# Kernel tuning notes

Measured on AMD Instinct MI355X. Metric: run time of the kernel, lower is better.

Reference implementation:

```python
import jax, jax.numpy as jnp
import numpy as np

N_STATE = 1024
N_HEADS = 16
D_HEAD = N_STATE // N_HEADS
N_CTX = 4080
T_PAD = 128 * 32  # ctx_blks * block_size = 4096
N_RESBLOCKS = 24
LN_EPS = 1e-5


def setup_inputs() -> dict:
    key = jax.random.key(0)
    ks = jax.random.split(key, 12)
    std_qkv = 1.0 / np.sqrt(N_STATE)
    std_c = 1.0 / np.sqrt(N_STATE * N_RESBLOCKS ** 2)
    return {
        "m": jax.random.normal(ks[0], (1, N_CTX, N_STATE), jnp.float32),
        "bias": jax.random.normal(ks[1], (T_PAD, T_PAD), jnp.float32) * 0.1,
        "gamma": jnp.ones((N_STATE,), jnp.float32),
        "beta": jnp.zeros((N_STATE,), jnp.float32),
        "Wq": jax.random.normal(ks[2], (N_STATE, N_STATE), jnp.float32) * std_qkv,
        "bq": jnp.zeros((N_STATE,), jnp.float32),
        "Wk": jax.random.normal(ks[3], (N_STATE, N_STATE), jnp.float32) * std_qkv,
        "Wv": jax.random.normal(ks[4], (N_STATE, N_STATE), jnp.float32) * std_qkv,
        "bv": jnp.zeros((N_STATE,), jnp.float32),
        "Wc": jax.random.normal(ks[5], (N_STATE, N_STATE), jnp.float32) * std_c,
        "bc": jnp.zeros((N_STATE,), jnp.float32),
    }


def reference(m, bias, gamma, beta, Wq, bq, Wk, Wv, bv, Wc, bc):
    B, n_ctx, n_state = m.shape
    n_pad = T_PAD - n_ctx  # same pad for queries and keys here

    # LayerNorm
    mu = jnp.mean(m, axis=-1, keepdims=True)
    var = jnp.mean(jnp.square(m - mu), axis=-1, keepdims=True)
    r = (m - mu) * jax.lax.rsqrt(var + LN_EPS) * gamma + beta

    q = r @ Wq + bq
    k = r @ Wk          # f_k has use_bias=False
    v = r @ Wv + bv

    pad = ((0, 0), (0, n_pad), (0, 0))
    q = jnp.pad(q, pad)
    k = jnp.pad(k, pad)
    v = jnp.pad(v, pad)

    # [B, T_PAD, H, D] -> attention per head
    q = q.reshape(B, T_PAD, N_HEADS, D_HEAD)
    k = k.reshape(B, T_PAD, N_HEADS, D_HEAD)
    v = v.reshape(B, T_PAD, N_HEADS, D_HEAD)

    scale = 1.0 / np.sqrt(D_HEAD)  # qk_scale; applied as sqrt(scale) to q and k
    w = jnp.einsum("bqhd,bkhd->bhqk", q, k) * scale  # [B,H,T_PAD,T_PAD]
    w = jax.nn.softmax(w + bias[None, None], axis=-1)

    r = jnp.einsum("bhqk,bkhd->bqhd", w, v).reshape(B, T_PAD, n_state)
    r = r[:, :n_ctx]
    r = r @ Wc + bc
    return m + r
```

## Files before the change

### kernel.cpp

```cpp
#include <hip/hip_runtime.h>
#include <hip/hip_bf16.h>

#define NCTX 4080
#define TPAD 4096
#define NS   1024
#define NH   16
#define DH   64

typedef __attribute__((ext_vector_type(8))) short short8;
typedef __attribute__((ext_vector_type(4))) float f32x4;
typedef unsigned short u16;
typedef unsigned int   u32;

#define MFMA(a,b,c) __builtin_amdgcn_mfma_f32_16x16x32_bf16(a,b,c,0,0,0)

__device__ __forceinline__ u16 f2bf(float f) {
  u32 u = __float_as_uint(f);
  u += 0x7fffu + ((u >> 16) & 1u);
  return (u16)(u >> 16);
}

__device__ __forceinline__ void gload16(const void* g, void* l) {
  __builtin_amdgcn_global_load_lds(
      (const __attribute__((address_space(1))) u32*)g,
      (__attribute__((address_space(3))) u32*)l, 16, 0, 0);
}

__global__ __launch_bounds__(256) void ln_kernel(const float* __restrict__ mm,
    const float* __restrict__ gamma, const float* __restrict__ beta,
    u16* __restrict__ r) {
  int row = blockIdx.x;
  int t = threadIdx.x;
  if (row >= NCTX) {
    ushort4 z; z.x = z.y = z.z = z.w = 0;
    *reinterpret_cast<ushort4*>(&r[(size_t)row*NS + t*4]) = z;
    return;
  }
  float4 x = *reinterpret_cast<const float4*>(&mm[(size_t)row*NS + t*4]);
  float s  = x.x + x.y + x.z + x.w;
  float ss = x.x*x.x + x.y*x.y + x.z*x.z + x.w*x.w;
  for (int off = 32; off > 0; off >>= 1) {
    s  += __shfl_down(s, off);
    ss += __shfl_down(ss, off);
  }
  __shared__ float red[2][4];
  int wid = t >> 6, lane = t & 63;
  if (lane == 0) { red[0][wid] = s; red[1][wid] = ss; }
  __syncthreads();
  s  = red[0][0] + red[0][1] + red[0][2] + red[0][3];
  ss = red[1][0] + red[1][1] + red[1][2] + red[1][3];
  float mu  = s * (1.f/NS);
  float var = ss * (1.f/NS) - mu*mu;
  float rs  = rsqrtf(var + 1e-5f);
  float4 g = *reinterpret_cast<const float4*>(&gamma[t*4]);
  float4 b = *reinterpret_cast<const float4*>(&beta[t*4]);
  ushort4 o;
  o.x = f2bf((x.x - mu)*rs*g.x + b.x);
  o.y = f2bf((x.y - mu)*rs*g.y + b.y);
  o.z = f2bf((x.z - mu)*rs*g.z + b.z);
  o.w = f2bf((x.w - mu)*rs*g.w + b.w);
  *reinterpret_cast<ushort4*>(&r[(size_t)row*NS + t*4]) = o;
}

__global__ __launch_bounds__(256) void wconv_kernel(const float* __restrict__ W0,
    const float* __restrict__ W1, const float* __restrict__ W2,
    const float* __restrict__ W3, u16* __restrict__ dstbase) {
  const float* srcs[4] = {W0, W1, W2, W3};
  const float* W = srcs[blockIdx.z];
  u16* dst = dstbase + (size_t)blockIdx.z * NS * NS;
  int k0 = blockIdx.x * 64, n0 = blockIdx.y * 64;
  __shared__ float tile[64][65];
  int t = threadIdx.x;
  int rr = t >> 4;
  int c4 = (t & 15) * 4;
  #pragma unroll
  for (int sb = 0; sb < 4; sb++) {
    int rowk = rr + sb*16;
    float4 v = *reinterpret_cast<const float4*>(&W[(size_t)(k0+rowk)*NS + n0 + c4]);
    tile[rowk][c4] = v.x; tile[rowk][c4+1] = v.y;
    tile[rowk][c4+2] = v.z; tile[rowk][c4+3] = v.w;
  }
  __syncthreads();
  #pragma unroll
  for (int sb = 0; sb < 4; sb++) {
    int nn = rr + sb*16;
    ushort4 o;
    o.x = f2bf(tile[c4  ][nn]);
    o.y = f2bf(tile[c4+1][nn]);
    o.z = f2bf(tile[c4+2][nn]);
    o.w = f2bf(tile[c4+3][nn]);
    *reinterpret_cast<ushort4*>(&dst[(size_t)(n0+nn)*NS + k0 + c4]) = o;
  }
}

__global__ __launch_bounds__(256) void gemm_qkv(const u16* __restrict__ A,
    const u16* __restrict__ wT, const float* __restrict__ bqp,
    const float* __restrict__ bvp, u16* __restrict__ qp, u16* __restrict__ kp,
    u16* __restrict__ vp) {
  int z = blockIdx.z;
  const u16* BT = wT + (size_t)z * (NS*NS);
  const float* bias = (z == 0) ? bqp : ((z == 2) ? bvp : nullptr);
  u16* C = (z == 0) ? qp : ((z == 1) ? kp : vp);
  float scale = (z == 0) ? 0.125f : 1.0f;
  int transOut = (z == 2);

  int m0 = blockIdx.x * 128, n0 = blockIdx.y * 128;
  int tid = threadIdx.x, lane = tid & 63, wid = tid >> 6;
  int l15 = lane & 15, g = lane >> 4;
  int wm = wid >> 1, wn = wid & 1;
  __shared__ u16 sA[2][128*32];
  __shared__ u16 sB[2][128*32];
  f32x4 acc[4][4] = {};

  auto stage = [&](int buf, int kt) {
    int k0 = kt * 32;
    #pragma unroll
    for (int s2 = 0; s2 < 2; s2++) {
      int T = s2*256 + tid;
      gload16(&A [(size_t)(m0 + (T>>2))*NS + k0 + (T&3)*8], &sA[buf][(s2*256 + wid*64)*8]);
    }
    #pragma unroll
    for (int s2 = 0; s2 < 2; s2++) {
      int T = s2*256 + tid;
      gload16(&BT[(size_t)(n0 + (T>>2))*NS + k0 + (T&3)*8], &sB[buf][(s2*256 + wid*64)*8]);
    }
  };
  auto compute = [&](int buf) {
    short8 af[4], bf_[4];
    #pragma unroll
    for (int i = 0; i < 4; i++)
      af[i] = *reinterpret_cast<const short8*>(&sA[buf][(wm*64 + i*16 + l15)*32 + g*8]);
    #pragma unroll
    for (int j = 0; j < 4; j++)
      bf_[j] = *reinterpret_cast<const short8*>(&sB[buf][(wn*64 + j*16 + l15)*32 + g*8]);
    #pragma unroll
    for (int i = 0; i < 4; i++)
      #pragma unroll
      for (int j = 0; j < 4; j++)
        acc[i][j] = MFMA(af[i], bf_[j], acc[i][j]);
  };

  stage(0, 0);
  __syncthreads();
  int cur = 0;
  for (int kt = 0; kt < 31; kt++) {
    stage(cur ^ 1, kt + 1);
    compute(cur);
    __syncthreads();
    cur ^= 1;
  }
  compute(cur);

  if (!transOut) {
    #pragma unroll
    for (int i = 0; i < 4; i++)
      #pragma unroll
      for (int r = 0; r < 4; r++) {
        int row = m0 + wm*64 + i*16 + g*4 + r;
        #pragma unroll
        for (int j = 0; j < 4; j++) {
          int col = n0 + wn*64 + j*16 + l15;
          float v = acc[i][j][r];
          if (bias && row < NCTX) v += bias[col];
          C[(size_t)row*NS + col] = f2bf(v * scale);
        }
      }
  } else {
    #pragma unroll
    for (int i = 0; i < 4; i++)
      #pragma unroll
      for (int j = 0; j < 4; j++) {
        int col  = n0 + wn*64 + j*16 + l15;
        int rowb = m0 + wm*64 + i*16 + g*4;
        u16 ov[4];
        #pragma unroll
        for (int r = 0; r < 4; r++) {
          float v = acc[i][j][r];
          if (bias && (rowb + r) < NCTX) v += bias[col];
          ov[r] = f2bf(v * scale);
        }
        ushort4 o; o.x = ov[0]; o.y = ov[1]; o.z = ov[2]; o.w = ov[3];
        *reinterpret_cast<ushort4*>(&C[(size_t)col*TPAD + rowb]) = o;
      }
  }
}

__global__ __launch_bounds__(256, 4) void attn_kernel(const u16* __restrict__ q,
    const u16* __restrict__ kp, const u16* __restrict__ vt,
    const float* __restrict__ bias, u16* __restrict__ ao) {
  int h  = blockIdx.x;
  int q0 = blockIdx.y * 64;
  int tid = threadIdx.x, lane = tid & 63, w = tid >> 6;
  int l15 = lane & 15, g = lane >> 4;
  int qr = q0 + w*16;

  __shared__ u16 sK[2][64][64];
  __shared__ u16 sP[4][16][72];

  auto stageK = [&](int buf, int kt) {
    int k0 = kt * 64;
    #pragma unroll
    for (int s2 = 0; s2 < 2; s2++) {
      int slot = s2*256 + tid;
      int row  = slot >> 3;
      int kb   = (slot & 7) << 4;
      int kbs  = kb ^ ((row & 7) << 4);
      gload16(&kp[(size_t)(k0 + row)*NS + h*DH + (kbs >> 1)],
              &sK[buf][0][0] + (size_t)(s2*256 + w*64)*8);
    }
  };

  short8 aq[2];
  aq[0] = *reinterpret_cast<const short8*>(&q[(size_t)(qr + l15)*NS + h*DH + g*8]);
  aq[1] = *reinterpret_cast<const short8*>(&q[(size_t)(qr + l15)*NS + h*DH + 32 + g*8]);

  f32x4 o[4] = {};
  float m = -1e30f, l = 0.f;

  stageK(0, 0);
  __syncthreads();

  for (int kt = 0; kt < 64; kt++) {
    int buf = kt & 1;
    if (kt < 63) stageK(buf ^ 1, kt + 1);
    int k0 = kt * 64;

    float4 bb[4];
    #pragma unroll
    for (int c = 0; c < 4; c++)
      bb[c] = *reinterpret_cast<const float4*>(
          &bias[(size_t)(qr + l15)*TPAD + k0 + c*16 + g*4]);

    f32x4 s[4];
    int sw = (l15 & 7) << 4;
    #pragma unroll
    for (int c = 0; c < 4; c++) {
      int rowl = c*16 + l15;
      short8 kf0 = *reinterpret_cast<const short8*>(&sK[buf][rowl][((g*16) ^ sw) >> 1]);
      short8 kf1 = *reinterpret_cast<const short8*>(&sK[buf][rowl][((64 + g*16) ^ sw) >> 1]);
      f32x4 t = {};
      t = MFMA(kf0, aq[0], t);
      t = MFMA(kf1, aq[1], t);
      s[c] = t;
    }

    short8 vf[4][2];
    #pragma unroll
    for (int d = 0; d < 4; d++)
      #pragma unroll
      for (int kc = 0; kc < 2; kc++)
        vf[d][kc] = *reinterpret_cast<const short8*>(
            &vt[(size_t)(h*DH + d*16 + l15)*TPAD + k0 + kc*32 + g*8]);

    #pragma unroll
    for (int c = 0; c < 4; c++) {
      s[c][0] += bb[c].x; s[c][1] += bb[c].y;
      s[c][2] += bb[c].z; s[c][3] += bb[c].w;
    }

    float pm = fmaxf(fmaxf(fmaxf(s[0][0], s[0][1]), fmaxf(s[0][2], s[0][3])),
                     fmaxf(fmaxf(s[1][0], s[1][1]), fmaxf(s[1][2], s[1][3])));
    pm = fmaxf(pm, fmaxf(fmaxf(fmaxf(s[2][0], s[2][1]), fmaxf(s[2][2], s[2][3])),
                         fmaxf(fmaxf(s[3][0], s[3][1]), fmaxf(s[3][2], s[3][3]))));
    pm = fmaxf(pm, __shfl_xor(pm, 16));
    pm = fmaxf(pm, __shfl_xor(pm, 32));
    float mn = fmaxf(m, pm);
    float cs = __expf(m - mn);
    m = mn;
    float rs = 0.f;
    #pragma unroll
    for (int c = 0; c < 4; c++)
      #pragma unroll
      for (int r = 0; r < 4; r++) {
        float p = __expf(s[c][r] - mn);
        s[c][r] = p;
        rs += p;
      }
    rs += __shfl_xor(rs, 16);
    rs += __shfl_xor(rs, 32);
    l = l*cs + rs;
    #pragma unroll
    for (int d = 0; d < 4; d++)
      #pragma unroll
      for (int r = 0; r < 4; r++)
        o[d][r] *= cs;

    #pragma unroll
    for (int c = 0; c < 4; c++) {
      u32 w0, w1;
      asm("v_cvt_pk_bf16_f32 %0, %1, %2" : "=v"(w0) : "v"(s[c][0]), "v"(s[c][1]));
      asm("v_cvt_pk_bf16_f32 %0, %1, %2" : "=v"(w1) : "v"(s[c][2]), "v"(s[c][3]));
      uint2 pw; pw.x = w0; pw.y = w1;
      *reinterpret_cast<uint2*>(&sP[w][l15][c*16 + g*4]) = pw;
    }

    short8 pa0 = *reinterpret_cast<const short8*>(&sP[w][l15][g*8]);
    short8 pa1 = *reinterpret_cast<const short8*>(&sP[w][l15][32 + g*8]);
    #pragma unroll
    for (int d = 0; d < 4; d++) {
      o[d] = MFMA(vf[d][0], pa0, o[d]);
      o[d] = MFMA(vf[d][1], pa1, o[d]);
    }
    __syncthreads();
  }

  float inv = 1.f / l;
  #pragma unroll
  for (int d = 0; d < 4; d++) {
    ushort4 ov;
    ov.x = f2bf(o[d][0] * inv);
    ov.y = f2bf(o[d][1] * inv);
    ov.z = f2bf(o[d][2] * inv);
    ov.w = f2bf(o[d][3] * inv);
    *reinterpret_cast<ushort4*>(
        &ao[(size_t)(qr + l15)*NS + h*DH + d*16 + g*4]) = ov;
  }
}

__global__ __launch_bounds__(256) void gemm_final(const u16* __restrict__ A,
    const u16* __restrict__ BT, const float* __restrict__ bc,
    const float* __restrict__ mm, float* __restrict__ out) {
  int m0 = blockIdx.x * 128, n0 = blockIdx.y * 128;
  int tid = threadIdx.x, lane = tid & 63, wid = tid >> 6;
  int l15 = lane & 15, g = lane >> 4;
  int wm = wid >> 1, wn = wid & 1;
  __shared__ u16 sA[2][128*32];
  __shared__ u16 sB[2][128*32];
  f32x4 acc[4][4] = {};

  auto stage = [&](int buf, int kt) {
    int k0 = kt * 32;
    #pragma unroll
    for (int s2 = 0; s2 < 2; s2++) {
      int T = s2*256 + tid;
      gload16(&A [(size_t)(m0 + (T>>2))*NS + k0 + (T&3)*8], &sA[buf][(s2*256 + wid*64)*8]);
    }
    #pragma unroll
    for (int s2 = 0; s2 < 2; s2++) {
      int T = s2*256 + tid;
      gload16(&BT[(size_t)(n0 + (T>>2))*NS + k0 + (T&3)*8], &sB[buf][(s2*256 + wid*64)*8]);
    }
  };
  auto compute = [&](int buf) {
    short8 af[4], bf_[4];
    #pragma unroll
    for (int i = 0; i < 4; i++)
      af[i] = *reinterpret_cast<const short8*>(&sA[buf][(wm*64 + i*16 + l15)*32 + g*8]);
    #pragma unroll
    for (int j = 0; j < 4; j++)
      bf_[j] = *reinterpret_cast<const short8*>(&sB[buf][(wn*64 + j*16 + l15)*32 + g*8]);
    #pragma unroll
    for (int i = 0; i < 4; i++)
      #pragma unroll
      for (int j = 0; j < 4; j++)
        acc[i][j] = MFMA(af[i], bf_[j], acc[i][j]);
  };

  stage(0, 0);
  __syncthreads();
  int cur = 0;
  for (int kt = 0; kt < 31; kt++) {
    stage(cur ^ 1, kt + 1);
    compute(cur);
    __syncthreads();
    cur ^= 1;
  }
  compute(cur);

  #pragma unroll
  for (int i = 0; i < 4; i++)
    #pragma unroll
    for (int r = 0; r < 4; r++) {
      int row = m0 + wm*64 + i*16 + g*4 + r;
      if (row >= NCTX) continue;
      #pragma unroll
      for (int j = 0; j < 4; j++) {
        int col = n0 + wn*64 + j*16 + l15;
        out[(size_t)row*NS + col] = acc[i][j][r] + bc[col] + mm[(size_t)row*NS + col];
      }
    }
}

extern "C" void kernel_launch(void* const* d_in, const int* in_sizes, int n_in,
                              void* d_out, int out_size, void* d_ws, size_t ws_size,
                              hipStream_t stream) {
  (void)in_sizes; (void)n_in; (void)out_size; (void)ws_size;
  const float* mm    = (const float*)d_in[0];
  const float* bias  = (const float*)d_in[1];
  const float* gamma = (const float*)d_in[2];
  const float* beta  = (const float*)d_in[3];
  const float* Wq    = (const float*)d_in[4];
  const float* bq    = (const float*)d_in[5];
  const float* Wk    = (const float*)d_in[6];
  const float* Wv    = (const float*)d_in[7];
  const float* bv    = (const float*)d_in[8];
  const float* Wc    = (const float*)d_in[9];
  const float* bc    = (const float*)d_in[10];

  char* ws = (char*)d_ws;
  const size_t MB = 1u << 20;
  u16* rbf = (u16*)(ws +  0*MB);
  u16* qbf = (u16*)(ws +  8*MB);
  u16* kbf = (u16*)(ws + 16*MB);
  u16* vtb = (u16*)(ws + 24*MB);
  u16* wT  = (u16*)(ws + 32*MB);
  u16* aob = (u16*)(ws + 40*MB);

  ln_kernel   <<<TPAD, 256, 0, stream>>>(mm, gamma, beta, rbf);
  wconv_kernel<<<dim3(16,16,4), 256, 0, stream>>>(Wq, Wk, Wv, Wc, wT);
  gemm_qkv    <<<dim3(32,8,3), 256, 0, stream>>>(rbf, wT, bq, bv, qbf, kbf, vtb);
  attn_kernel <<<dim3(NH,64), 256, 0, stream>>>(qbf, kbf, vtb, bias, aob);
  gemm_final  <<<dim3(32,8), 256, 0, stream>>>(aob, wT + 3*(NS*NS), bc, mm, (float*)d_out);
}
```

Measured before the change: 564.8 us.

## Split attention over two key halves and merge partial softmax results

Splits the attention key range into two halves across a third grid dimension, so each block runs 32 key tiles and writes unnormalized bf16 partial outputs plus its running max and sum. A new merge kernel combines the two halves with the usual log-sum-exp rescaling before the output projection. The bias tile is now loaded one iteration ahead, V loads are moved earlier in the loop, and the occupancy hint is raised from 4 to 5. The goal is more blocks in flight to fill the GPU and better hiding of load latency. The cost is an extra kernel launch, extra partial-output traffic, and the precision loss of storing unnormalized partials in bf16.

```diff
diff --git a/kernel.cpp b/kernel.cpp
--- a/kernel.cpp
+++ b/kernel.cpp
@@ -185,11 +185,13 @@
   }
 }
 
-__global__ __launch_bounds__(256, 4) void attn_kernel(const u16* __restrict__ q,
+__global__ __launch_bounds__(256, 5) void attn_kernel(const u16* __restrict__ q,
     const u16* __restrict__ kp, const u16* __restrict__ vt,
-    const float* __restrict__ bias, u16* __restrict__ ao) {
-  int h  = blockIdx.x;
-  int q0 = blockIdx.y * 64;
+    const float* __restrict__ bias, u16* __restrict__ op, float* __restrict__ ml) {
+  int h    = blockIdx.x;
+  int q0   = blockIdx.y * 64;
+  int half = blockIdx.z;
+  int kbase = half * 2048;
   int tid = threadIdx.x, lane = tid & 63, w = tid >> 6;
   int l15 = lane & 15, g = lane >> 4;
   int qr = q0 + w*16;
@@ -198,7 +200,7 @@
   __shared__ u16 sP[4][16][72];
 
   auto stageK = [&](int buf, int kt) {
-    int k0 = kt * 64;
+    int k0 = kbase + kt * 64;
     #pragma unroll
     for (int s2 = 0; s2 < 2; s2++) {
       int slot = s2*256 + tid;
@@ -210,6 +212,14 @@
     }
   };
 
+  const float* brow = &bias[(size_t)(qr + l15)*TPAD + kbase];
+  auto loadBias = [&](int kt, float4* bb) {
+    int k0 = kt * 64;
+    #pragma unroll
+    for (int c = 0; c < 4; c++)
+      bb[c] = *reinterpret_cast<const float4*>(&brow[k0 + c*16 + g*4]);
+  };
+
   short8 aq[2];
   aq[0] = *reinterpret_cast<const short8*>(&q[(size_t)(qr + l15)*NS + h*DH + g*8]);
   aq[1] = *reinterpret_cast<const short8*>(&q[(size_t)(qr + l15)*NS + h*DH + 32 + g*8]);
@@ -217,19 +227,26 @@
   f32x4 o[4] = {};
   float m = -1e30f, l = 0.f;
 
+  float4 bb[4];
+  loadBias(0, bb);
   stageK(0, 0);
   __syncthreads();
 
-  for (int kt = 0; kt < 64; kt++) {
+  for (int kt = 0; kt < 32; kt++) {
     int buf = kt & 1;
-    if (kt < 63) stageK(buf ^ 1, kt + 1);
-    int k0 = kt * 64;
-
-    float4 bb[4];
-    #pragma unroll
-    for (int c = 0; c < 4; c++)
-      bb[c] = *reinterpret_cast<const float4*>(
-          &bias[(size_t)(qr + l15)*TPAD + k0 + c*16 + g*4]);
+    if (kt < 31) stageK(buf ^ 1, kt + 1);
+    int k0 = kbase + kt * 64;
+
+    float4 bn[4];
+    loadBias((kt + 1) & 31, bn);
+
+    short8 vf[4][2];
+    #pragma unroll
+    for (int d = 0; d < 4; d++)
+      #pragma unroll
+      for (int kc = 0; kc < 2; kc++)
+        vf[d][kc] = *reinterpret_cast<const short8*>(
+            &vt[(size_t)(h*DH + d*16 + l15)*TPAD + k0 + kc*32 + g*8]);
 
     f32x4 s[4];
     int sw = (l15 & 7) << 4;
@@ -243,14 +260,6 @@
       t = MFMA(kf1, aq[1], t);
       s[c] = t;
     }
-
-    short8 vf[4][2];
-    #pragma unroll
-    for (int d = 0; d < 4; d++)
-      #pragma unroll
-      for (int kc = 0; kc < 2; kc++)
-        vf[d][kc] = *reinterpret_cast<const short8*>(
-            &vt[(size_t)(h*DH + d*16 + l15)*TPAD + k0 + kc*32 + g*8]);
 
     #pragma unroll
     for (int c = 0; c < 4; c++) {
@@ -301,20 +310,45 @@
       o[d] = MFMA(vf[d][0], pa0, o[d]);
       o[d] = MFMA(vf[d][1], pa1, o[d]);
     }
+
+    #pragma unroll
+    for (int c = 0; c < 4; c++) bb[c] = bn[c];
     __syncthreads();
   }
 
-  float inv = 1.f / l;
   #pragma unroll
   for (int d = 0; d < 4; d++) {
     ushort4 ov;
-    ov.x = f2bf(o[d][0] * inv);
-    ov.y = f2bf(o[d][1] * inv);
-    ov.z = f2bf(o[d][2] * inv);
-    ov.w = f2bf(o[d][3] * inv);
+    ov.x = f2bf(o[d][0]); ov.y = f2bf(o[d][1]);
+    ov.z = f2bf(o[d][2]); ov.w = f2bf(o[d][3]);
     *reinterpret_cast<ushort4*>(
-        &ao[(size_t)(qr + l15)*NS + h*DH + d*16 + g*4]) = ov;
-  }
+        &op[(size_t)(half*TPAD + qr + l15)*NS + h*DH + d*16 + g*4]) = ov;
+  }
+  if (g == 0) {
+    float2 v; v.x = m; v.y = l;
+    *reinterpret_cast<float2*>(&ml[((size_t)(half*NH + h)*TPAD + qr + l15)*2]) = v;
+  }
+}
+
+__global__ __launch_bounds__(256) void merge_kernel(const u16* __restrict__ op,
+    const float* __restrict__ ml, u16* __restrict__ ao) {
+  int qrow = blockIdx.x;
+  int t = threadIdx.x;
+  int col = t * 4;
+  int h = col >> 6;
+  float2 ml0 = *reinterpret_cast<const float2*>(&ml[((size_t)h*TPAD + qrow)*2]);
+  float2 ml1 = *reinterpret_cast<const float2*>(&ml[((size_t)(NH + h)*TPAD + qrow)*2]);
+  float M  = fmaxf(ml0.x, ml1.x);
+  float w0 = __expf(ml0.x - M), w1 = __expf(ml1.x - M);
+  float inv = 1.f / (ml0.y*w0 + ml1.y*w1);
+  ushort4 a = *reinterpret_cast<const ushort4*>(&op[(size_t)qrow*NS + col]);
+  ushort4 b = *reinterpret_cast<const ushort4*>(&op[(size_t)(TPAD + qrow)*NS + col]);
+  ushort4 r;
+  r.x = f2bf((__uint_as_float((u32)a.x << 16)*w0 + __uint_as_float((u32)b.x << 16)*w1)*inv);
+  r.y = f2bf((__uint_as_float((u32)a.y << 16)*w0 + __uint_as_float((u32)b.y << 16)*w1)*inv);
+  r.z = f2bf((__uint_as_float((u32)a.z << 16)*w0 + __uint_as_float((u32)b.z << 16)*w1)*inv);
+  r.w = f2bf((__uint_as_float((u32)a.w << 16)*w0 + __uint_as_float((u32)b.w << 16)*w1)*inv);
+  *reinterpret_cast<ushort4*>(&ao[(size_t)qrow*NS + col]) = r;
 }
 
 __global__ __launch_bounds__(256) void gemm_final(const u16* __restrict__ A,
@@ -399,16 +433,19 @@
 
   char* ws = (char*)d_ws;
   const size_t MB = 1u << 20;
-  u16* rbf = (u16*)(ws +  0*MB);
-  u16* qbf = (u16*)(ws +  8*MB);
-  u16* kbf = (u16*)(ws + 16*MB);
-  u16* vtb = (u16*)(ws + 24*MB);
-  u16* wT  = (u16*)(ws + 32*MB);
-  u16* aob = (u16*)(ws + 40*MB);
+  u16*   rbf = (u16*)(ws +  0*MB);
+  u16*   qbf = (u16*)(ws +  8*MB);
+  u16*   kbf = (u16*)(ws + 16*MB);
+  u16*   vtb = (u16*)(ws + 24*MB);
+  u16*   wT  = (u16*)(ws + 32*MB);
+  u16*   aob = (u16*)(ws + 40*MB);
+  u16*   opb = (u16*)(ws + 48*MB);
+  float* mlb = (float*)(ws + 64*MB);
 
   ln_kernel   <<<TPAD, 256, 0, stream>>>(mm, gamma, beta, rbf);
   wconv_kernel<<<dim3(16,16,4), 256, 0, stream>>>(Wq, Wk, Wv, Wc, wT);
   gemm_qkv    <<<dim3(32,8,3), 256, 0, stream>>>(rbf, wT, bq, bv, qbf, kbf, vtb);
-  attn_kernel <<<dim3(NH,64), 256, 0, stream>>>(qbf, kbf, vtb, bias, aob);
+  attn_kernel <<<dim3(NH,64,2), 256, 0, stream>>>(qbf, kbf, vtb, bias, opb, mlb);
+  merge_kernel<<<TPAD, 256, 0, stream>>>(opb, mlb, aob);
   gemm_final  <<<dim3(32,8), 256, 0, stream>>>(aob, wT + 3*(NS*NS), bc, mm, (float*)d_out);
 }
```

After: 619.0 us. +9.6%, slower.
